# Kernel optimization log

Hardware: AMD Instinct MI355X
Metric: run time of the kernel (lower is better)

The kernel has to match this reference:

```python
import jax, jax.numpy as jnp
import numpy as np

DX = 1.0
DY = 1.0
W_DIV = 1e9
W_SMOOTH = 10.0
W_STD = 100.0
EPS = 1e-10


def _corner(a, i, j, k):
    # slice dims 2,3,4: 0 -> [0:-1], 1 -> [1:]
    sl = lambda b: slice(1, None) if b else slice(0, -1)
    return a[:, :, sl(i), sl(j), sl(k)]


def setup_inputs() -> dict:
    key = jax.random.key(0)
    k1, k2 = jax.random.split(key)
    outputs = jax.random.normal(k1, (2, 1, 256, 256, 64), dtype=jnp.float32)
    targets = jax.random.normal(k2, (2, 3, 256, 256, 64), dtype=jnp.float32)
    return {"outputs": outputs, "targets": targets}


def _loss(outputs, targets):
    bx, by, bz = targets[:, 0:1], targets[:, 1:2], targets[:, 2:3]
    z = outputs[:, 0:1]

    # vertical thickness and smoothness of its square
    dz = z[..., 1:] - z[..., :-1]
    dz2 = dz ** 2
    lap = (6 * dz2[:, :, 1:-1, 1:-1, 1:-1]
           - dz2[:, :, :-2, 1:-1, 1:-1] - dz2[:, :, 2:, 1:-1, 1:-1]
           - dz2[:, :, 1:-1, :-2, 1:-1] - dz2[:, :, 1:-1, 2:, 1:-1]
           - dz2[:, :, 1:-1, 1:-1, 2:] - dz2[:, :, 1:-1, 1:-1, :-2])
    loss_smooth = jnp.mean(lap ** 2)

    # per-(batch, channel, z) std over the spatial plane (unbiased, matching torch.std)
    loss_std = jnp.mean(jnp.std(dz, axis=(2, 3), ddof=1))

    # 8 cell corners for each field
    corners = lambda a: {(i, j, k): _corner(a, i, j, k)
                         for i in (0, 1) for j in (0, 1) for k in (0, 1)}
    BX, BY, BZ, Z = corners(bx), corners(by), corners(bz), corners(z)

    az = lambda a, b: jnp.abs(Z[a] - Z[b])
    num = (0.25 * (BX[1,0,0] + BX[1,1,0] + BX[1,0,1] + BX[1,1,1]) * DY * 0.5 * (az((1,0,1),(1,0,0)) + az((1,1,1),(1,1,0)))
           - 0.25 * (BX[0,0,0] + BX[0,1,0] + BX[0,0,1] + BX[0,1,1]) * DY * 0.5 * (az((0,0,1),(0,0,0)) + az((0,1,1),(0,1,0)))
           + 0.25 * (BY[0,1,0] + BY[1,1,0] + BY[0,1,1] + BY[1,1,1]) * DX * 0.5 * (az((0,1,1),(0,1,0)) + az((1,1,1),(1,1,0)))
           - 0.25 * (BY[0,0,0] + BY[1,0,0] + BY[0,0,1] + BY[1,0,1]) * DX * 0.5 * (az((0,0,1),(0,0,0)) + az((1,0,1),(1,0,0)))
           + 0.25 * (BZ[0,0,1] + BZ[0,1,1] + BZ[1,0,1] + BZ[1,1,1]) * DX * DY
           - 0.25 * (BZ[0,0,0] + BZ[0,1,0] + BZ[1,0,0] + BZ[1,1,0]) * DX * DY
           + (BX[0,0,1] + BX[1,0,1] + BX[1,1,1]) * DY * (Z[0,0,1] - Z[1,0,1]) / 6
           + (BX[0,1,1] + BX[1,1,1] + BX[1,0,1]) * DY * (Z[0,1,1] - Z[1,1,1]) / 6
           + (BY[1,0,1] + BY[1,1,1] + BY[0,1,1]) * DX * (Z[1,0,1] - Z[1,1,1]) / 6
           + (BY[0,0,1] + BY[0,1,1] + BY[1,1,1]) * DX * (Z[0,0,1] - Z[0,1,1]) / 6
           - (BX[0,0,0] + BX[1,0,0] + BX[1,1,0]) * DY * (Z[0,0,0] - Z[1,0,0]) / 6
           - (BX[0,1,0] + BX[1,1,0] + BX[1,0,0]) * DY * (Z[0,1,0] - Z[1,1,0]) / 6
           - (BY[1,0,0] + BY[1,1,0] + BY[0,1,0]) * DX * (Z[1,0,0] - Z[1,1,0]) / 6
           - (BY[0,0,0] + BY[0,1,0] + BY[1,1,0]) * DX * (Z[0,0,0] - Z[0,1,0]) / 6)

    sum8 = lambda C: sum(C.values())
    den = ((sum8(BX) * 0.125) ** 2 + (sum8(BY) * 0.125) ** 2
           + (sum8(BZ) * 0.125) ** 2 + EPS)
    loss_div = jnp.mean(num ** 2 / den)

    return loss_div * W_DIV, loss_smooth * W_SMOOTH + loss_std * W_STD


def reference(outputs, targets):
    return _loss(outputs, targets)
```

## Files before the change

kernel.cpp:

```cpp
#include <hip/hip_runtime.h>
#include <math.h>


#define XSF 16384

__global__ __launch_bounds__(512) void zero_ws_kernel(float* ws) {
    for (int i = threadIdx.x; i < 32 * 258; i += 512) ws[i] = 0.0f;
}

__device__ __forceinline__ void ld5(float* a, const float* p, int d4) {
    float4 x = *(const float4*)p;
    float4 y = *(const float4*)(p + d4);
    a[0] = x.x; a[1] = x.y; a[2] = x.z; a[3] = x.w; a[4] = y.x;
}

__global__ __launch_bounds__(256, 3) void fused_loss_kernel(
    const float* __restrict__ zin, const float* __restrict__ tg,
    float* __restrict__ ws)
{
    __shared__ float r1[1024];
    __shared__ float r2[1024];
    __shared__ float rsc[4][2];

    const int tid  = threadIdx.x;
    const int lane = tid & 63;
    const int w    = tid >> 6;

    const int virt = ((blockIdx.x & 7) << 10) | (blockIdx.x >> 3);
    const int bb   = virt >> 12;
    const int rest = virt & 4095;
    const int x0 = ((rest >> 6) & 63) << 2;
    const int y0 = (rest & 63) << 2;

    const int c  = tid >> 4;
    const int kq = tid & 15;
    const int cx = c & 3, cy = c >> 2;
    const int xg = x0 + cx, yg = y0 + cy;
    const int k0 = kq << 2;

    const bool interior = (x0 >= 4) && (x0 <= 248) && (y0 >= 4) && (y0 <= 248);

    const int oC = xg * XSF + yg * 64 + k0;
    int oE, oW, oN, oS, oNE, d4;
    if (interior) {
        oE = oC + XSF; oW = oC - XSF; oN = oC + 64; oS = oC - 64; oNE = oC + XSF + 64;
        d4 = 4;
    } else {
        const int xE = (xg < 255) ? xg + 1 : 255;
        const int xW = (xg > 0)   ? xg - 1 : 0;
        const int yN = (yg < 255) ? yg + 1 : 255;
        const int yS = (yg > 0)   ? yg - 1 : 0;
        oE  = xE * XSF + yg * 64 + k0;
        oW  = xW * XSF + yg * 64 + k0;
        oN  = xg * XSF + yN * 64 + k0;
        oS  = xg * XSF + yS * 64 + k0;
        oNE = xE * XSF + yN * 64 + k0;
        d4  = (kq < 15) ? 4 : 0;
    }

    const float* zg  = zin + ((size_t)bb << 22);
    const float* bxg = tg  + ((size_t)(bb * 3) << 22);
    const float* byg = bxg + (1u << 22);
    const float* bzg = byg + (1u << 22);

    float zcv[7];
    {
        int km = (k0 >= 4) ? -4 : 0;
        float4 m = *(const float4*)&zg[oC + km];
        float4 a = *(const float4*)&zg[oC];
        float4 b = *(const float4*)&zg[oC + d4];
        zcv[0] = m.w; zcv[1] = a.x; zcv[2] = a.y; zcv[3] = a.z; zcv[4] = a.w;
        zcv[5] = b.x; zcv[6] = b.y;
    }
    float zEv[5], zWv[5], zNv[5], zSv[5], zNEv[5];
    ld5(zEv,  &zg[oE],  d4);
    ld5(zWv,  &zg[oW],  d4);
    ld5(zNv,  &zg[oN],  d4);
    ld5(zSv,  &zg[oS],  d4);
    ld5(zNEv, &zg[oNE], d4);

    float X00[5], X10[5], X01[5], X11[5];
    ld5(X00, &bxg[oC], d4);  ld5(X10, &bxg[oE], d4);
    ld5(X01, &bxg[oN], d4);  ld5(X11, &bxg[oNE], d4);
    float Y00[5], Y10[5], Y01[5], Y11[5];
    ld5(Y00, &byg[oC], d4);  ld5(Y10, &byg[oE], d4);
    ld5(Y01, &byg[oN], d4);  ld5(Y11, &byg[oNE], d4);
    float Z00[5], Z10[5], Z01[5], Z11[5];
    ld5(Z00, &bzg[oC], d4);  ld5(Z10, &bzg[oE], d4);
    ld5(Z01, &bzg[oN], d4);  ld5(Z11, &bzg[oNE], d4);

    float dz0[4], dzE[4], dzN[4], dzNE[4];
    #pragma unroll
    for (int e = 0; e < 4; ++e) {
        dz0[e]  = zcv[e + 2] - zcv[e + 1];
        dzE[e]  = zEv[e + 1] - zEv[e];
        dzN[e]  = zNv[e + 1] - zNv[e];
        dzNE[e] = zNEv[e + 1] - zNEv[e];
    }
    float s1a[4], s2a[4];
    #pragma unroll
    for (int e = 0; e < 4; ++e) {
        bool kok = (k0 + e) < 63;
        s1a[e] = kok ? dz0[e] : 0.0f;
        s2a[e] = kok ? dz0[e] * dz0[e] : 0.0f;
    }

    float sm = 0.0f;
    if (xg >= 1 && xg <= 254 && yg >= 1 && yg <= 254) {
        #pragma unroll
        for (int e = 0; e < 4; ++e) {
            int k = k0 + e;
            if (k >= 1 && k <= 61) {
                float dzm = zcv[e + 1] - zcv[e];
                float dzp = zcv[e + 3] - zcv[e + 2];
                float dzw = zWv[e + 1] - zWv[e];
                float dzs = zSv[e + 1] - zSv[e];
                float lap = 6.0f * dz0[e] * dz0[e]
                          - dzw * dzw - dzE[e] * dzE[e]
                          - dzs * dzs - dzN[e] * dzN[e]
                          - dzm * dzm - dzp * dzp;
                sm += lap * lap;
            }
        }
    }

    float dv = 0.0f;
    if (xg < 255 && yg < 255) {
        float dCE[5], dCN[5], dENE[5], dNNE[5];
        #pragma unroll
        for (int j = 0; j < 5; ++j) {
            dCE[j]  = zcv[j + 1] - zEv[j];
            dCN[j]  = zcv[j + 1] - zNv[j];
            dENE[j] = zEv[j] - zNEv[j];
            dNNE[j] = zNv[j] - zNEv[j];
        }
        float sxp[4], sxm[4], syp[4], sym[4];
        #pragma unroll
        for (int e = 0; e < 4; ++e) {
            float aC = fabsf(dz0[e]),  aE  = fabsf(dzE[e]);
            float aN = fabsf(dzN[e]),  aNE = fabsf(dzNE[e]);
            sxp[e] = aE + aNE;  sxm[e] = aC + aN;
            syp[e] = aN + aNE;  sym[e] = aC + aE;
        }

        const float c6 = 1.0f / 6.0f;
        float num[4], den[4];

        {
            float qx[5], px2[5], g[5];
            #pragma unroll
            for (int j = 0; j < 5; ++j) {
                qx[j]  = X10[j] + X11[j];
                px2[j] = X00[j] + X01[j];
                g[j]   = (qx[j] + X00[j]) * dCE[j] + (qx[j] + X01[j]) * dNNE[j];
            }
            #pragma unroll
            for (int e = 0; e < 4; ++e) {
                float qq = qx[e] + qx[e + 1], pp = px2[e] + px2[e + 1];
                num[e] = 0.125f * (qq * sxp[e] - pp * sxm[e]) + c6 * (g[e + 1] - g[e]);
                float s = qq + pp;
                den[e] = s * s;
            }
        }
        {
            float qy[5], py2[5], h[5];
            #pragma unroll
            for (int j = 0; j < 5; ++j) {
                qy[j]  = Y01[j] + Y11[j];
                py2[j] = Y00[j] + Y10[j];
                h[j]   = (qy[j] + Y10[j]) * dENE[j] + (qy[j] + Y00[j]) * dCN[j];
            }
            #pragma unroll
            for (int e = 0; e < 4; ++e) {
                float qq = qy[e] + qy[e + 1], pp = py2[e] + py2[e + 1];
                num[e] += 0.125f * (qq * syp[e] - pp * sym[e]) + c6 * (h[e + 1] - h[e]);
                float s = qq + pp;
                den[e] += s * s;
            }
        }
        {
            float sz[5];
            #pragma unroll
            for (int j = 0; j < 5; ++j)
                sz[j] = Z00[j] + Z10[j] + Z01[j] + Z11[j];
            #pragma unroll
            for (int e = 0; e < 4; ++e) {
                num[e] += 0.25f * (sz[e + 1] - sz[e]);
                float s = sz[e] + sz[e + 1];
                den[e] += s * s;
            }
        }
        #pragma unroll
        for (int e = 0; e < 4; ++e) {
            if ((k0 + e) < 63) {
                float d = den[e] * 0.015625f + 1e-10f;
                dv += num[e] * num[e] * __builtin_amdgcn_rcpf(d);
            }
        }
    }

    #pragma unroll
    for (int off = 32; off > 0; off >>= 1) {
        sm += __shfl_down(sm, off, 64);
        dv += __shfl_down(dv, off, 64);
    }

    { float4 v; v.x = s1a[0]; v.y = s1a[1]; v.z = s1a[2]; v.w = s1a[3];
      *(float4*)&r1[tid << 2] = v; }
    { float4 v; v.x = s2a[0]; v.y = s2a[1]; v.z = s2a[2]; v.w = s2a[3];
      *(float4*)&r2[tid << 2] = v; }
    if (lane == 0) { rsc[w][0] = sm; rsc[w][1] = dv; }
    __syncthreads();

    if (tid < 64) {
        float a = 0.0f, b2 = 0.0f;
        #pragma unroll
        for (int cc = 0; cc < 16; ++cc) {
            a  += r1[cc * 64 + tid];
            b2 += r2[cc * 64 + tid];
        }
        float* sl = ws + (blockIdx.x & 31) * 258;
        if (tid < 63) {
            atomicAdd(&sl[2 + bb * 64 + tid],   a);
            atomicAdd(&sl[130 + bb * 64 + tid], b2);
        }
        if (tid == 0) atomicAdd(&sl[0], rsc[0][0] + rsc[1][0] + rsc[2][0] + rsc[3][0]);
        if (tid == 1) atomicAdd(&sl[1], rsc[0][1] + rsc[1][1] + rsc[2][1] + rsc[3][1]);
    }
}

__global__ __launch_bounds__(128) void finalize_kernel(const float* __restrict__ ws,
                                                       float* __restrict__ out)
{
    __shared__ double red[128];
    const int t = threadIdx.x;
    double stdv = 0.0;
    {
        int k = t & 63, bb = t >> 6;
        if (k < 63) {
            double s1 = 0.0, s2 = 0.0;
            for (int p = 0; p < 32; ++p) {
                s1 += (double)ws[p * 258 + 2 + bb * 64 + k];
                s2 += (double)ws[p * 258 + 130 + bb * 64 + k];
            }
            const double N = 65536.0;
            double var = (s2 - s1 * s1 / N) / (N - 1.0);
            stdv = sqrt(var > 0.0 ? var : 0.0);
        }
    }
    red[t] = stdv;
    __syncthreads();
    for (int off = 64; off > 0; off >>= 1) {
        if (t < off) red[t] += red[t + off];
        __syncthreads();
    }
    if (t == 0) {
        double smt = 0.0, dvt = 0.0;
        for (int p = 0; p < 32; ++p) {
            smt += (double)ws[p * 258 + 0];
            dvt += (double)ws[p * 258 + 1];
        }
        double loss_std    = red[0] / 126.0;
        double loss_smooth = smt / (2.0 * 254.0 * 254.0 * 61.0);
        double loss_div    = dvt / (2.0 * 255.0 * 255.0 * 63.0);
        out[0] = (float)(loss_div * 1e9);
        out[1] = (float)(loss_smooth * 10.0 + loss_std * 100.0);
    }
}

extern "C" void kernel_launch(void* const* d_in, const int* in_sizes, int n_in,
                              void* d_out, int out_size, void* d_ws, size_t ws_size,
                              hipStream_t stream) {
    const float* z  = (const float*)d_in[0];
    const float* tg = (const float*)d_in[1];
    float* out = (float*)d_out;
    float* ws  = (float*)d_ws;

    zero_ws_kernel<<<1, 512, 0, stream>>>(ws);
    fused_loss_kernel<<<8192, 256, 0, stream>>>(z, tg, ws);
    finalize_kernel<<<1, 128, 0, stream>>>(ws, out);
}
```

Before: 216.1 us.

## Stage z and B-field halo tiles in shared memory before stencil compute

```diff
diff --git a/kernel.cpp b/kernel.cpp
--- a/kernel.cpp
+++ b/kernel.cpp
@@ -2,24 +2,23 @@
 #include <math.h>
 
 
-#define XSF 16384
+#define RS 68
 
 __global__ __launch_bounds__(512) void zero_ws_kernel(float* ws) {
     for (int i = threadIdx.x; i < 32 * 258; i += 512) ws[i] = 0.0f;
 }
 
-__device__ __forceinline__ void ld5(float* a, const float* p, int d4) {
+__device__ __forceinline__ void ld5(float* a, const float* p) {
     float4 x = *(const float4*)p;
-    float4 y = *(const float4*)(p + d4);
-    a[0] = x.x; a[1] = x.y; a[2] = x.z; a[3] = x.w; a[4] = y.x;
-}
-
-__global__ __launch_bounds__(256, 3) void fused_loss_kernel(
+    a[0] = x.x; a[1] = x.y; a[2] = x.z; a[3] = x.w; a[4] = p[4];
+}
+
+__global__ __launch_bounds__(256) void fused_loss_kernel(
     const float* __restrict__ zin, const float* __restrict__ tg,
     float* __restrict__ ws)
 {
-    __shared__ float r1[1024];
-    __shared__ float r2[1024];
+    __shared__ float zs[36 * RS];
+    __shared__ float bs[75 * RS];
     __shared__ float rsc[4][2];
 
     const int tid  = threadIdx.x;
@@ -32,62 +31,51 @@
     const int x0 = ((rest >> 6) & 63) << 2;
     const int y0 = (rest & 63) << 2;
 
+    const float* zg = zin + ((size_t)bb << 22);
+
+    for (int i = tid; i < 1776; i += 256) {
+        int r = i >> 4, o = (i & 15) << 2;
+        const float* src;
+        float* dst;
+        if (r < 36) {
+            int xi = r / 6, yr = r - xi * 6;
+            int x = x0 - 1 + xi; x = x < 0 ? 0 : (x > 255 ? 255 : x);
+            int y = y0 - 1 + yr; y = y < 0 ? 0 : (y > 255 ? 255 : y);
+            src = &zg[x * 16384 + y * 64 + o];
+            dst = &zs[r * RS + o];
+        } else {
+            int rr = r - 36;
+            int f = rr / 25, rem = rr - f * 25;
+            int xi = rem / 5, yr = rem - xi * 5;
+            int x = x0 + xi; x = x > 255 ? 255 : x;
+            int y = y0 + yr; y = y > 255 ? 255 : y;
+            src = &tg[((size_t)(bb * 3 + f) << 22) + x * 16384 + y * 64 + o];
+            dst = &bs[rr * RS + o];
+        }
+        *(float4*)dst = *(const float4*)src;
+    }
+    __syncthreads();
+
     const int c  = tid >> 4;
     const int kq = tid & 15;
     const int cx = c & 3, cy = c >> 2;
     const int xg = x0 + cx, yg = y0 + cy;
     const int k0 = kq << 2;
 
-    const bool interior = (x0 >= 4) && (x0 <= 248) && (y0 >= 4) && (y0 <= 248);
-
-    const int oC = xg * XSF + yg * 64 + k0;
-    int oE, oW, oN, oS, oNE, d4;
-    if (interior) {
-        oE = oC + XSF; oW = oC - XSF; oN = oC + 64; oS = oC - 64; oNE = oC + XSF + 64;
-        d4 = 4;
-    } else {
-        const int xE = (xg < 255) ? xg + 1 : 255;
-        const int xW = (xg > 0)   ? xg - 1 : 0;
-        const int yN = (yg < 255) ? yg + 1 : 255;
-        const int yS = (yg > 0)   ? yg - 1 : 0;
-        oE  = xE * XSF + yg * 64 + k0;
-        oW  = xW * XSF + yg * 64 + k0;
-        oN  = xg * XSF + yN * 64 + k0;
-        oS  = xg * XSF + yS * 64 + k0;
-        oNE = xE * XSF + yN * 64 + k0;
-        d4  = (kq < 15) ? 4 : 0;
-    }
-
-    const float* zg  = zin + ((size_t)bb << 22);
-    const float* bxg = tg  + ((size_t)(bb * 3) << 22);
-    const float* byg = bxg + (1u << 22);
-    const float* bzg = byg + (1u << 22);
+    const float* zC = &zs[((cx + 1) * 6 + (cy + 1)) * RS + k0];
 
     float zcv[7];
     {
-        int km = (k0 >= 4) ? -4 : 0;
-        float4 m = *(const float4*)&zg[oC + km];
-        float4 a = *(const float4*)&zg[oC];
-        float4 b = *(const float4*)&zg[oC + d4];
-        zcv[0] = m.w; zcv[1] = a.x; zcv[2] = a.y; zcv[3] = a.z; zcv[4] = a.w;
-        zcv[5] = b.x; zcv[6] = b.y;
+        float4 a = *(const float4*)zC;
+        zcv[0] = zC[-1]; zcv[1] = a.x; zcv[2] = a.y; zcv[3] = a.z; zcv[4] = a.w;
+        zcv[5] = zC[4];  zcv[6] = zC[5];
     }
     float zEv[5], zWv[5], zNv[5], zSv[5], zNEv[5];
-    ld5(zEv,  &zg[oE],  d4);
-    ld5(zWv,  &zg[oW],  d4);
-    ld5(zNv,  &zg[oN],  d4);
-    ld5(zSv,  &zg[oS],  d4);
-    ld5(zNEv, &zg[oNE], d4);
-
-    float X00[5], X10[5], X01[5], X11[5];
-    ld5(X00, &bxg[oC], d4);  ld5(X10, &bxg[oE], d4);
-    ld5(X01, &bxg[oN], d4);  ld5(X11, &bxg[oNE], d4);
-    float Y00[5], Y10[5], Y01[5], Y11[5];
-    ld5(Y00, &byg[oC], d4);  ld5(Y10, &byg[oE], d4);
-    ld5(Y01, &byg[oN], d4);  ld5(Y11, &byg[oNE], d4);
-    float Z00[5], Z10[5], Z01[5], Z11[5];
-    ld5(Z00, &bzg[oC], d4);  ld5(Z10, &bzg[oE], d4);
-    ld5(Z01, &bzg[oN], d4);  ld5(Z11, &bzg[oNE], d4);
+    ld5(zEv,  zC + 6 * RS);
+    ld5(zWv,  zC - 6 * RS);
+    ld5(zNv,  zC + RS);
+    ld5(zSv,  zC - RS);
+    ld5(zNEv, zC + 7 * RS);
 
     float dz0[4], dzE[4], dzN[4], dzNE[4];
     #pragma unroll
@@ -143,16 +131,20 @@
             syp[e] = aN + aNE;  sym[e] = aC + aE;
         }
 
+        const float* bP = &bs[(cx * 5 + cy) * RS + k0];
         const float c6 = 1.0f / 6.0f;
         float num[4], den[4];
 
         {
+            float A00[5], A10[5], A01[5], A11[5];
+            ld5(A00, bP);                ld5(A10, bP + 5 * RS);
+            ld5(A01, bP + RS);           ld5(A11, bP + 6 * RS);
             float qx[5], px2[5], g[5];
             #pragma unroll
             for (int j = 0; j < 5; ++j) {
-                qx[j]  = X10[j] + X11[j];
-                px2[j] = X00[j] + X01[j];
-                g[j]   = (qx[j] + X00[j]) * dCE[j] + (qx[j] + X01[j]) * dNNE[j];
+                qx[j]  = A10[j] + A11[j];
+                px2[j] = A00[j] + A01[j];
+                g[j]   = (qx[j] + A00[j]) * dCE[j] + (qx[j] + A01[j]) * dNNE[j];
             }
             #pragma unroll
             for (int e = 0; e < 4; ++e) {
@@ -163,12 +155,16 @@
             }
         }
         {
+            const float* bQ = bP + 25 * RS;
+            float A00[5], A10[5], A01[5], A11[5];
+            ld5(A00, bQ);                ld5(A10, bQ + 5 * RS);
+            ld5(A01, bQ + RS);           ld5(A11, bQ + 6 * RS);
             float qy[5], py2[5], h[5];
             #pragma unroll
             for (int j = 0; j < 5; ++j) {
-                qy[j]  = Y01[j] + Y11[j];
-                py2[j] = Y00[j] + Y10[j];
-                h[j]   = (qy[j] + Y10[j]) * dENE[j] + (qy[j] + Y00[j]) * dCN[j];
+                qy[j]  = A01[j] + A11[j];
+                py2[j] = A00[j] + A10[j];
+                h[j]   = (qy[j] + A10[j]) * dENE[j] + (qy[j] + A00[j]) * dCN[j];
             }
             #pragma unroll
             for (int e = 0; e < 4; ++e) {
@@ -179,10 +175,14 @@
             }
         }
         {
+            const float* bR = bP + 50 * RS;
+            float A00[5], A10[5], A01[5], A11[5];
+            ld5(A00, bR);                ld5(A10, bR + 5 * RS);
+            ld5(A01, bR + RS);           ld5(A11, bR + 6 * RS);
             float sz[5];
             #pragma unroll
             for (int j = 0; j < 5; ++j)
-                sz[j] = Z00[j] + Z10[j] + Z01[j] + Z11[j];
+                sz[j] = A00[j] + A10[j] + A01[j] + A11[j];
             #pragma unroll
             for (int e = 0; e < 4; ++e) {
                 num[e] += 0.25f * (sz[e + 1] - sz[e]);
@@ -205,6 +205,9 @@
         dv += __shfl_down(dv, off, 64);
     }
 
+    __syncthreads();
+    float* r1 = zs;
+    float* r2 = zs + 1024;
     { float4 v; v.x = s1a[0]; v.y = s1a[1]; v.z = s1a[2]; v.w = s1a[3];
       *(float4*)&r1[tid << 2] = v; }
     { float4 v; v.x = s2a[0]; v.y = s2a[1]; v.z = s2a[2]; v.w = s2a[3];
```

After: 207.6 us. 1.04x faster.
